# Kernel optimization log

Measured on AMD Instinct MI355X. Metric: run time of the kernel, lower is better.

Reference implementation:

```python
import jax, jax.numpy as jnp
import numpy as np

B, T, D, H = 2, 2048, 1024, 4
DK, DV = 1024, 2048          # key_dim = d_model*expand_k, value_dim = d_model*expand_v
HK, HV = DK // H, DV // H    # 256, 512 per-head dims
LR = 16                      # gate_low_rank_dim
EPS = 1e-5
GATE_NORM = 16.0             # gate_logit_normalizer


def _xavier(k, shape, gain):
    fan_in, fan_out = shape
    lim = gain * np.sqrt(6.0 / (fan_in + fan_out))
    return jax.random.uniform(k, shape, jnp.float32, -lim, lim)


def setup_inputs() -> dict:
    key = jax.random.key(0)
    ks = jax.random.split(key, 10)
    g_qkv = 2 ** (-2.5)
    return {
        "x": jax.random.normal(ks[0], (B, T, D), jnp.float32),
        "Wq": _xavier(ks[1], (D, DK), g_qkv),
        "Wk": _xavier(ks[2], (D, DK), g_qkv),
        "Wv": _xavier(ks[3], (D, DV), g_qkv),
        "Wg": _xavier(ks[4], (D, DV), g_qkv),
        "gk_w1": _xavier(ks[5], (D, LR), g_qkv),
        "gk_w2": _xavier(ks[6], (LR, DK), g_qkv),
        "gk_b": jnp.zeros((DK,), jnp.float32),
        "Wo": _xavier(ks[7], (DV, D), 2 ** (-1)),
        "rms_w": jnp.ones((HV,), jnp.float32),
    }


def _gla_scan(q, k, v, g):
    # q,k,g: [T, hk]; v: [T, hv]. Recurrence S_t = diag(exp(g_t)) S_{t-1} + k_t v_t^T; o_t = q_t @ S_t
    S0 = jnp.zeros((q.shape[-1], v.shape[-1]), q.dtype)

    def step(S, inp):
        qt, kt, vt, gt = inp
        S = jnp.exp(gt)[:, None] * S + kt[:, None] * vt[None, :]
        return S, qt @ S

    return jax.lax.scan(step, S0, (q, k, v, g))[1]  # [T, hv]


def _forward(x, Wq, Wk, Wv, Wg, gk_w1, gk_w2, gk_b, Wo, rms_w):
    b, t = x.shape[0], x.shape[1]
    scale = HK ** -0.5
    # projections -> [b, h, t, d_head]
    q = (x @ Wq).reshape(b, t, H, HK).transpose(0, 2, 1, 3) * scale
    k = (x @ Wk).reshape(b, t, H, HK).transpose(0, 2, 1, 3)
    v = (x @ Wv).reshape(b, t, H, HV).transpose(0, 2, 1, 3)
    # low-rank forget gate, log-space, fp32
    gl = (x @ gk_w1) @ gk_w2 + gk_b
    g = (jax.nn.log_sigmoid(gl.astype(jnp.float32)) / GATE_NORM)
    g = g.reshape(b, t, H, HK).transpose(0, 2, 1, 3)
    # per-(batch, head) linear-attention recurrence
    o = jax.vmap(jax.vmap(_gla_scan))(q, k, v, g)  # [b, h, t, hv]
    # group RMSNorm over head_v_dim
    o = o.transpose(0, 2, 1, 3)  # [b, t, h, hv]
    o = o * jax.lax.rsqrt(jnp.mean(o * o, axis=-1, keepdims=True) + EPS) * rms_w
    # output gate (swish) + out projection
    o = o.reshape(b, t, DV) * jax.nn.silu(x @ Wg)
    return o @ Wo  # [b, t, d_model]


def reference(x, Wq, Wk, Wv, Wg, gk_w1, gk_w2, gk_b, Wo, rms_w):
    return _forward(x, Wq, Wk, Wv, Wg, gk_w1, gk_w2, gk_b, Wo, rms_w)
```

## Files before the change

kernel.cpp:

```cpp
#include <hip/hip_runtime.h>
#include <cstdint>
#include <cstddef>


typedef unsigned short u16;
typedef __attribute__((ext_vector_type(8))) short s8v;
typedef __attribute__((ext_vector_type(4))) float f4v;

__device__ __forceinline__ u16 f2b(float f) {
  unsigned u = __builtin_bit_cast(unsigned, f);
  unsigned r = u + 0x7FFFu + ((u >> 16) & 1u);
  return (u16)(r >> 16);
}
__device__ __forceinline__ float b2f(u16 h) {
  unsigned u = ((unsigned)h) << 16;
  return __builtin_bit_cast(float, u);
}

__device__ __forceinline__ void cp16(const void* g, void* l) {
  __builtin_amdgcn_global_load_lds(
      (const __attribute__((address_space(1))) unsigned int*)g,
      (__attribute__((address_space(3))) unsigned int*)l, 16, 0, 0);
}

__device__ __forceinline__ void stage_tile(const u16* g, int ld, u16* lds,
                                           int wv, int ln) {
#pragma unroll
  for (int i = 0; i < 2; ++i) {
    const int c = wv * 2 + i;
    const u16* src = g + (size_t)(c * 16 + (ln >> 2)) * ld + (ln & 3) * 8;
    cp16(src, lds + c * 512);
  }
}

__device__ __forceinline__ void gemm_core(
    const u16* __restrict__ A, int lda, const u16* __restrict__ BT, int ldb,
    int K, u16* As, u16* Bs, f4v acc[4][4])
{
  const int tid = threadIdx.x;
  const int ln = tid & 63, wv = tid >> 6;
  const int arow = (wv >> 1) * 64 + (ln & 15);
  const int brow = (wv & 1) * 64 + (ln & 15);
  const int kq = (ln >> 4) * 8;
  const int nt = K >> 5;
  stage_tile(A, lda, As, wv, ln);
  stage_tile(BT, ldb, Bs, wv, ln);
  stage_tile(A + 32, lda, As + 4096, wv, ln);
  stage_tile(BT + 32, ldb, Bs + 4096, wv, ln);
  stage_tile(A + 64, lda, As + 8192, wv, ln);
  stage_tile(BT + 64, ldb, Bs + 8192, wv, ln);
  int slot = 0;
  for (int t = 0; t < nt; ++t) {
    const int rem = nt - 1 - t;
    if (rem >= 2)      asm volatile("s_waitcnt vmcnt(8)" ::: "memory");
    else if (rem == 1) asm volatile("s_waitcnt vmcnt(4)" ::: "memory");
    else               asm volatile("s_waitcnt vmcnt(0)" ::: "memory");
    __builtin_amdgcn_s_barrier();
    __builtin_amdgcn_sched_barrier(0);
    const u16* Ab = As + slot * 4096;
    const u16* Bb = Bs + slot * 4096;
    s8v af[4], bf[4];
#pragma unroll
    for (int f = 0; f < 4; ++f)
      af[f] = *(const s8v*)(Ab + (arow + f * 16) * 32 + kq);
#pragma unroll
    for (int f = 0; f < 4; ++f)
      bf[f] = *(const s8v*)(Bb + (brow + f * 16) * 32 + kq);
#pragma unroll
    for (int mf = 0; mf < 4; ++mf)
#pragma unroll
      for (int nf = 0; nf < 4; ++nf)
        acc[mf][nf] = __builtin_amdgcn_mfma_f32_16x16x32_bf16(
            af[mf], bf[nf], acc[mf][nf], 0, 0, 0);
    __builtin_amdgcn_sched_barrier(0);
    __builtin_amdgcn_s_barrier();
    if (t + 3 < nt) {
      stage_tile(A + (t + 3) * 32, lda, As + slot * 4096, wv, ln);
      stage_tile(BT + (t + 3) * 32, ldb, Bs + slot * 4096, wv, ln);
    }
    slot = (slot == 2) ? 0 : slot + 1;
  }
}

#define EPI_SETUP                                            \
  const int tid = threadIdx.x;                               \
  const int ln = tid & 63, wv = tid >> 6;                    \
  const int wr = wv >> 1, wc = wv & 1;

#define ZERO_ACC(acc)                                        \
  _Pragma("unroll")                                          \
  for (int zi = 0; zi < 4; ++zi)                             \
    _Pragma("unroll")                                        \
    for (int zj = 0; zj < 4; ++zj)                           \
      acc[zi][zj] = (f4v){0.f, 0.f, 0.f, 0.f};

__global__ __launch_bounds__(256) void cast_b(const float* __restrict__ in,
                                              u16* __restrict__ out) {
  const int i = blockIdx.x * 256 + threadIdx.x;
  const float4 v = ((const float4*)in)[i];
  u16* p = out + i * 4;
  p[0] = f2b(v.x); p[1] = f2b(v.y); p[2] = f2b(v.z); p[3] = f2b(v.w);
}

__global__ __launch_bounds__(256) void wtrans(const float* __restrict__ in,
                                              u16* __restrict__ out, int R, int C) {
  __shared__ float t[32][33];
  const int c0 = blockIdx.x * 32, r0 = blockIdx.y * 32;
  const int lx = threadIdx.x & 31, ly = threadIdx.x >> 5;
#pragma unroll
  for (int i = 0; i < 32; i += 8)
    t[ly + i][lx] = in[(size_t)(r0 + ly + i) * C + c0 + lx];
  __syncthreads();
#pragma unroll
  for (int i = 0; i < 32; i += 8)
    out[(size_t)(c0 + ly + i) * R + r0 + lx] = f2b(t[lx][ly + i]);
}

__global__ __launch_bounds__(256) void trans_b16(const u16* __restrict__ in,
                                                 u16* __restrict__ out, int R, int C) {
  __shared__ u16 t[32][33];
  const size_t boff = (size_t)blockIdx.z * R * C;
  const int c0 = blockIdx.x * 32, r0 = blockIdx.y * 32;
  const int lx = threadIdx.x & 31, ly = threadIdx.x >> 5;
#pragma unroll
  for (int i = 0; i < 32; i += 8)
    t[ly + i][lx] = in[boff + (size_t)(r0 + ly + i) * C + c0 + lx];
  __syncthreads();
#pragma unroll
  for (int i = 0; i < 32; i += 8)
    out[boff + (size_t)(c0 + ly + i) * R + r0 + lx] = t[lx][ly + i];
}

__global__ __launch_bounds__(256) void lowrank1(
    const float* __restrict__ x, const float* __restrict__ w1,
    float* __restrict__ tmp)
{
  const int idx = blockIdx.x * 256 + threadIdx.x;
  const int m = idx >> 4, i = idx & 15;
  const float* xr = x + (size_t)m * 1024;
  float acc = 0.f;
#pragma unroll 4
  for (int kk = 0; kk < 1024; kk += 4) {
    const float4 xv = *(const float4*)(xr + kk);
    acc = fmaf(xv.x, w1[(kk + 0) * 16 + i], acc);
    acc = fmaf(xv.y, w1[(kk + 1) * 16 + i], acc);
    acc = fmaf(xv.z, w1[(kk + 2) * 16 + i], acc);
    acc = fmaf(xv.w, w1[(kk + 3) * 16 + i], acc);
  }
  tmp[idx] = acc;
}

__global__ __launch_bounds__(256) void gate_cum(
    const float* __restrict__ tmp, const float* __restrict__ w2,
    const float* __restrict__ bias, u16* __restrict__ dq, u16* __restrict__ dk,
    float* __restrict__ Dc)
{
  __shared__ float ls_t[2048];
  const int b = blockIdx.y >> 4, c = blockIdx.y & 15;
  const int h = blockIdx.x;
  const int i = threadIdx.x;
  const int n = h * 256 + i;
  const int bh = b * 4 + h;
  const float* tp = tmp + ((size_t)(b * 2048 + c * 128)) * 16;
#pragma unroll
  for (int r = 0; r < 8; ++r) ls_t[r * 256 + threadIdx.x] = tp[r * 256 + threadIdx.x];
  __syncthreads();
  float w2c[16];
#pragma unroll
  for (int r = 0; r < 16; ++r) w2c[r] = w2[r * 1024 + n];
  const float bn = bias[n];
  const size_t base = ((size_t)bh * 2048 + c * 128) * 256 + i;
  float B = 0.f;
  for (int t = 0; t < 128; ++t) {
    float gl = bn;
    const float* tr = ls_t + t * 16;
#pragma unroll
    for (int r = 0; r < 16; ++r) gl = fmaf(tr[r], w2c[r], gl);
    const float ls = fminf(gl, 0.f) - log1pf(expf(-fabsf(gl)));
    B += ls * 0.0625f;
    const float eB = expf(B);
    dq[base + (size_t)t * 256] = f2b(eB);
    dk[base + (size_t)t * 256] = f2b(1.f / eB);
  }
  Dc[(bh * 16 + c) * 256 + i] = expf(B);
}

__global__ __launch_bounds__(256) void proj_all(
    const u16* __restrict__ xb, const u16* __restrict__ WT,
    const u16* __restrict__ dq, const u16* __restrict__ dk,
    u16* __restrict__ qt, u16* __restrict__ kt,
    u16* __restrict__ vr, u16* __restrict__ gpre)
{
  __shared__ __align__(16) u16 As[12288], Bs[12288];
  const int id = blockIdx.x;
  const int xcd = id & 7, j = id >> 3;
  const int m0 = (j / 6) * 128;
  const int n0 = (xcd * 6 + (j % 6)) * 128;
  f4v acc[4][4];
  ZERO_ACC(acc)
  gemm_core(xb + (size_t)m0 * 1024, 1024, WT + (size_t)n0 * 1024, 1024, 1024,
            As, Bs, acc);
  EPI_SETUP
#pragma unroll
  for (int mf = 0; mf < 4; ++mf)
#pragma unroll
    for (int nf = 0; nf < 4; ++nf)
#pragma unroll
      for (int r = 0; r < 4; ++r) {
        const int m = m0 + wr * 64 + mf * 16 + ((ln >> 4) << 2) + r;
        const int n = n0 + wc * 64 + nf * 16 + (ln & 15);
        const float val = acc[mf][nf][r];
        const int b = m >> 11, t = m & 2047;
        if (n0 < 1024) {
          const int bh = b * 4 + (n >> 8), i = n & 255;
          const size_t off = ((size_t)bh * 2048 + t) * 256 + i;
          qt[off] = f2b(val * 0.0625f * b2f(dq[off]));
        } else if (n0 < 2048) {
          const int nn = n - 1024;
          const int bh = b * 4 + (nn >> 8), i = nn & 255;
          const size_t off = ((size_t)bh * 2048 + t) * 256 + i;
          kt[off] = f2b(val * b2f(dk[off]));
        } else if (n0 < 4096) {
          const int nn = n - 2048;
          const int bh = b * 4 + (nn >> 9), jj = nn & 511;
          vr[((size_t)bh * 2048 + t) * 512 + jj] = f2b(val);
        } else {
          gpre[(size_t)m * 2048 + (n - 4096)] = f2b(val);
        }
      }
}

__global__ __launch_bounds__(256) void scan_gemms(
    const u16* __restrict__ vT, const u16* __restrict__ ktT,
    const u16* __restrict__ qt, const u16* __restrict__ kt,
    u16* __restrict__ UT, u16* __restrict__ Aw)
{
  __shared__ __align__(16) u16 As[12288], Bs[12288];
  const int bhc = blockIdx.y, bh = bhc >> 4, c = bhc & 15;
  f4v acc[4][4];
  ZERO_ACC(acc)
  if (blockIdx.x < 8) {
    const int mt = blockIdx.x >> 1, nt = blockIdx.x & 1;
    gemm_core(vT + ((size_t)bh * 512 + mt * 128) * 2048 + c * 128, 2048,
              ktT + ((size_t)bh * 256 + nt * 128) * 2048 + c * 128, 2048, 128,
              As, Bs, acc);
    EPI_SETUP
#pragma unroll
    for (int mf = 0; mf < 4; ++mf)
#pragma unroll
      for (int nf = 0; nf < 4; ++nf)
#pragma unroll
        for (int r = 0; r < 4; ++r) {
          const int j = mt * 128 + wr * 64 + mf * 16 + ((ln >> 4) << 2) + r;
          const int i = nt * 128 + wc * 64 + nf * 16 + (ln & 15);
          UT[(((size_t)(bh * 512 + j)) * 16 + c) * 256 + i] = f2b(acc[mf][nf][r]);
        }
  } else {
    const size_t base = ((size_t)bh * 2048 + c * 128) * 256;
    gemm_core(qt + base, 256, kt + base, 256, 256, As, Bs, acc);
    EPI_SETUP
    u16* Ap = Aw + (size_t)bhc * 16384;
#pragma unroll
    for (int mf = 0; mf < 4; ++mf)
#pragma unroll
      for (int nf = 0; nf < 4; ++nf)
#pragma unroll
        for (int r = 0; r < 4; ++r) {
          const int t = wr * 64 + mf * 16 + ((ln >> 4) << 2) + r;
          const int s = wc * 64 + nf * 16 + (ln & 15);
          Ap[t * 128 + s] = (s <= t) ? f2b(acc[mf][nf][r]) : (u16)0;
        }
  }
}

__global__ __launch_bounds__(256) void state_scan(
    u16* __restrict__ UT, const float* __restrict__ Dc)
{
  const int blk = blockIdx.x;
  const int bh = blk >> 9, j = blk & 511;
  const int i = threadIdx.x;
  u16* Up = UT + ((size_t)(bh * 512 + j)) * 16 * 256 + i;
  const float* Dp = Dc + bh * 16 * 256 + i;
  float S = 0.f;
  for (int c = 0; c < 16; ++c) {
    const float u = b2f(Up[c * 256]);
    Up[c * 256] = f2b(S);
    S = Dp[c * 256] * (S + u);
  }
}

__global__ __launch_bounds__(256) void intra_k(
    const u16* __restrict__ Aw, const u16* __restrict__ qt,
    const u16* __restrict__ vT, const u16* __restrict__ UT, u16* __restrict__ ob)
{
  __shared__ __align__(16) u16 As[12288], Bs[12288];
  const int jt = blockIdx.x;
  const int bhc = blockIdx.y, bh = bhc >> 4, c = bhc & 15;
  f4v acc[4][4];
  ZERO_ACC(acc)
  gemm_core(Aw + (size_t)bhc * 16384, 128,
            vT + ((size_t)bh * 512 + jt * 128) * 2048 + c * 128, 2048, 128,
            As, Bs, acc);
  gemm_core(qt + ((size_t)bh * 2048 + c * 128) * 256, 256,
            UT + ((size_t)(bh * 512 + jt * 128)) * 4096 + (size_t)c * 256, 4096, 256,
            As, Bs, acc);
  EPI_SETUP
  const int b = bh >> 2, h = bh & 3;
#pragma unroll
  for (int mf = 0; mf < 4; ++mf)
#pragma unroll
    for (int nf = 0; nf < 4; ++nf)
#pragma unroll
      for (int r = 0; r < 4; ++r) {
        const int t = c * 128 + wr * 64 + mf * 16 + ((ln >> 4) << 2) + r;
        const int j = jt * 128 + wc * 64 + nf * 16 + (ln & 15);
        ob[((size_t)(b * 2048 + t)) * 2048 + h * 512 + j] = f2b(acc[mf][nf][r]);
      }
}

__global__ __launch_bounds__(256) void rms_silu(
    u16* __restrict__ o, const u16* __restrict__ gpre, const float* __restrict__ w)
{
  const int grp = blockIdx.x * 4 + (threadIdx.x >> 6);
  const int lane = threadIdx.x & 63;
  const size_t base = (size_t)(grp >> 2) * 2048 + (grp & 3) * 512;
  float xv[8];
  float ss = 0.f;
#pragma unroll
  for (int i = 0; i < 8; ++i) {
    xv[i] = b2f(o[base + i * 64 + lane]);
    ss = fmaf(xv[i], xv[i], ss);
  }
#pragma unroll
  for (int off = 1; off < 64; off <<= 1) ss += __shfl_xor(ss, off, 64);
  const float r = rsqrtf(ss * (1.f / 512.f) + 1e-5f);
#pragma unroll
  for (int i = 0; i < 8; ++i) {
    const int cidx = i * 64 + lane;
    const float gp = b2f(gpre[base + cidx]);
    const float sig = 1.f / (1.f + expf(-gp));
    o[base + cidx] = f2b(xv[i] * r * w[cidx] * gp * sig);
  }
}

__global__ __launch_bounds__(256) void gemm_out(
    const u16* __restrict__ ob, const u16* __restrict__ WoT,
    float* __restrict__ pout)
{
  __shared__ __align__(16) u16 As[12288], Bs[12288];
  const int id = blockIdx.x;
  const int wg = (id & 7) * 64 + (id >> 3);
  const int ks = wg >> 8;
  const int tt = wg & 255;
  const int m0 = (tt & 31) * 128, n0 = (tt >> 5) * 128;
  f4v acc[4][4];
  ZERO_ACC(acc)
  gemm_core(ob + (size_t)m0 * 2048 + ks * 1024, 2048,
            WoT + (size_t)n0 * 2048 + ks * 1024, 2048, 1024, As, Bs, acc);
  EPI_SETUP
  float* po = pout + (size_t)ks * 4194304;
#pragma unroll
  for (int mf = 0; mf < 4; ++mf)
#pragma unroll
    for (int nf = 0; nf < 4; ++nf)
#pragma unroll
      for (int r = 0; r < 4; ++r) {
        const int m = m0 + wr * 64 + mf * 16 + ((ln >> 4) << 2) + r;
        const int n = n0 + wc * 64 + nf * 16 + (ln & 15);
        po[(size_t)m * 1024 + n] = acc[mf][nf][r];
      }
}

__global__ __launch_bounds__(256) void reduce_out(
    const float* __restrict__ p, float* __restrict__ out)
{
  const int i = blockIdx.x * 256 + threadIdx.x;
  const float4 a = ((const float4*)p)[i];
  const float4 b = ((const float4*)(p + 4194304))[i];
  ((float4*)out)[i] = make_float4(a.x + b.x, a.y + b.y, a.z + b.z, a.w + b.w);
}

extern "C" void kernel_launch(void* const* d_in, const int* in_sizes, int n_in,
                              void* d_out, int out_size, void* d_ws, size_t ws_size,
                              hipStream_t stream) {
  const float* x    = (const float*)d_in[0];
  const float* Wq   = (const float*)d_in[1];
  const float* Wk   = (const float*)d_in[2];
  const float* Wv   = (const float*)d_in[3];
  const float* Wg   = (const float*)d_in[4];
  const float* w1   = (const float*)d_in[5];
  const float* w2   = (const float*)d_in[6];
  const float* gb   = (const float*)d_in[7];
  const float* Wo   = (const float*)d_in[8];
  const float* rmsw = (const float*)d_in[9];
  float* out = (float*)d_out;

  char* W = (char*)d_ws;
  u16*   xb   = (u16*)W;   W += (size_t)8  << 20;
  u16*   WTa  = (u16*)W;   W += (size_t)12 << 20;
  u16*   WoT  = (u16*)W;   W += (size_t)4  << 20;
  u16*   qt   = (u16*)W;   W += (size_t)8  << 20;
  u16*   kt   = (u16*)W;   W += (size_t)8  << 20;
  u16*   vr   = (u16*)W;   W += (size_t)16 << 20;
  u16*   vT   = (u16*)W;   W += (size_t)16 << 20;
  u16*   ktT  = (u16*)W;   W += (size_t)8  << 20;
  u16*   gpre = (u16*)W;   W += (size_t)16 << 20;
  float* tmp  = (float*)W; W += (size_t)256 << 10;
  float* Dc   = (float*)W; W += (size_t)128 << 10;
  u16*   dq   = (u16*)W;   W += (size_t)8  << 20;
  u16*   dk   = (u16*)W;   W += (size_t)8  << 20;
  u16*   UT   = (u16*)W;   W += (size_t)32 << 20;
  u16*   Aw   = (u16*)W;   W += (size_t)4  << 20;
  u16*   ob   = (u16*)W;   W += (size_t)16 << 20;
  float* pout = (float*)W; W += (size_t)32 << 20;

  hipLaunchKernelGGL(lowrank1, dim3(256), dim3(256), 0, stream, x, w1, tmp);
  hipLaunchKernelGGL(gate_cum, dim3(4, 32), dim3(256), 0, stream,
                     tmp, w2, gb, dq, dk, Dc);

  hipLaunchKernelGGL(cast_b, dim3(4096), dim3(256), 0, stream, x, xb);
  hipLaunchKernelGGL(wtrans, dim3(32, 32), dim3(256), 0, stream, Wq, WTa, 1024, 1024);
  hipLaunchKernelGGL(wtrans, dim3(32, 32), dim3(256), 0, stream, Wk, WTa + 1048576, 1024, 1024);
  hipLaunchKernelGGL(wtrans, dim3(64, 32), dim3(256), 0, stream, Wv, WTa + 2097152, 1024, 2048);
  hipLaunchKernelGGL(wtrans, dim3(64, 32), dim3(256), 0, stream, Wg, WTa + 4194304, 1024, 2048);
  hipLaunchKernelGGL(wtrans, dim3(32, 64), dim3(256), 0, stream, Wo, WoT, 2048, 1024);

  hipLaunchKernelGGL(proj_all, dim3(1536), dim3(256), 0, stream,
                     xb, WTa, dq, dk, qt, kt, vr, gpre);

  hipLaunchKernelGGL(trans_b16, dim3(8, 64, 8), dim3(256), 0, stream,
                     kt, ktT, 2048, 256);
  hipLaunchKernelGGL(trans_b16, dim3(16, 64, 8), dim3(256), 0, stream,
                     vr, vT, 2048, 512);

  hipLaunchKernelGGL(scan_gemms, dim3(9, 128), dim3(256), 0, stream,
                     vT, ktT, qt, kt, UT, Aw);
  hipLaunchKernelGGL(state_scan, dim3(4096), dim3(256), 0, stream, UT, Dc);
  hipLaunchKernelGGL(intra_k, dim3(4, 128), dim3(256), 0, stream, Aw, qt, vT, UT, ob);

  hipLaunchKernelGGL(rms_silu, dim3(4096), dim3(256), 0, stream, ob, gpre, rmsw);
  hipLaunchKernelGGL(gemm_out, dim3(512), dim3(256), 0, stream, ob, WoT, pout);
  hipLaunchKernelGGL(reduce_out, dim3(4096), dim3(256), 0, stream, pout, out);
}
```

Baseline: 317.6 us.

## Swizzle GEMM LDS tiles and merge transpose launches into single kernels

The GEMM staging now permutes 16-byte chunks within each 32-element LDS row with an XOR swizzle, and the fragment reads use the matching swizzled offset. This is meant to cut LDS bank conflicts on the MFMA operand loads. Separately, the five weight-transpose launches and the two bf16 transpose launches are each folded into one kernel that dispatches on block index, which removes per-launch overhead. The swizzle has to agree exactly between the global-to-LDS copy and the reads, or the results will be wrong.

```diff
diff --git a/kernel.cpp b/kernel.cpp
--- a/kernel.cpp
+++ b/kernel.cpp
@@ -25,10 +25,11 @@
 
 __device__ __forceinline__ void stage_tile(const u16* g, int ld, u16* lds,
                                            int wv, int ln) {
+  const int q = (ln & 3) ^ ((ln >> 3) & 3);
 #pragma unroll
   for (int i = 0; i < 2; ++i) {
     const int c = wv * 2 + i;
-    const u16* src = g + (size_t)(c * 16 + (ln >> 2)) * ld + (ln & 3) * 8;
+    const u16* src = g + (size_t)(c * 16 + (ln >> 2)) * ld + q * 8;
     cp16(src, lds + c * 512);
   }
 }
@@ -41,7 +42,7 @@
   const int ln = tid & 63, wv = tid >> 6;
   const int arow = (wv >> 1) * 64 + (ln & 15);
   const int brow = (wv & 1) * 64 + (ln & 15);
-  const int kq = (ln >> 4) * 8;
+  const int koff = (((ln >> 4) ^ ((ln >> 1) & 3)) * 8);
   const int nt = K >> 5;
   stage_tile(A, lda, As, wv, ln);
   stage_tile(BT, ldb, Bs, wv, ln);
@@ -62,10 +63,10 @@
     s8v af[4], bf[4];
 #pragma unroll
     for (int f = 0; f < 4; ++f)
-      af[f] = *(const s8v*)(Ab + (arow + f * 16) * 32 + kq);
+      af[f] = *(const s8v*)(Ab + (arow + f * 16) * 32 + koff);
 #pragma unroll
     for (int f = 0; f < 4; ++f)
-      bf[f] = *(const s8v*)(Bb + (brow + f * 16) * 32 + kq);
+      bf[f] = *(const s8v*)(Bb + (brow + f * 16) * 32 + koff);
 #pragma unroll
     for (int mf = 0; mf < 4; ++mf)
 #pragma unroll
@@ -102,25 +103,43 @@
   p[0] = f2b(v.x); p[1] = f2b(v.y); p[2] = f2b(v.z); p[3] = f2b(v.w);
 }
 
-__global__ __launch_bounds__(256) void wtrans(const float* __restrict__ in,
-                                              u16* __restrict__ out, int R, int C) {
+__global__ __launch_bounds__(256) void wtrans_all(
+    const float* __restrict__ Wq, const float* __restrict__ Wk,
+    const float* __restrict__ Wv, const float* __restrict__ Wg,
+    const float* __restrict__ Wo, u16* __restrict__ WTa, u16* __restrict__ WoT)
+{
   __shared__ float t[32][33];
-  const int c0 = blockIdx.x * 32, r0 = blockIdx.y * 32;
+  const int id = blockIdx.x;
+  const float* src; u16* dst; int R, C, local;
+  if (id < 1024)      { src = Wq; dst = WTa;           R = 1024; C = 1024; local = id; }
+  else if (id < 2048) { src = Wk; dst = WTa + 1048576; R = 1024; C = 1024; local = id - 1024; }
+  else if (id < 4096) { src = Wv; dst = WTa + 2097152; R = 1024; C = 2048; local = id - 2048; }
+  else if (id < 6144) { src = Wg; dst = WTa + 4194304; R = 1024; C = 2048; local = id - 4096; }
+  else                { src = Wo; dst = WoT;           R = 2048; C = 1024; local = id - 6144; }
+  const int nx = C >> 5;
+  const int c0 = (local % nx) * 32, r0 = (local / nx) * 32;
   const int lx = threadIdx.x & 31, ly = threadIdx.x >> 5;
 #pragma unroll
   for (int i = 0; i < 32; i += 8)
-    t[ly + i][lx] = in[(size_t)(r0 + ly + i) * C + c0 + lx];
+    t[ly + i][lx] = src[(size_t)(r0 + ly + i) * C + c0 + lx];
   __syncthreads();
 #pragma unroll
   for (int i = 0; i < 32; i += 8)
-    out[(size_t)(c0 + ly + i) * R + r0 + lx] = f2b(t[lx][ly + i]);
-}
-
-__global__ __launch_bounds__(256) void trans_b16(const u16* __restrict__ in,
-                                                 u16* __restrict__ out, int R, int C) {
+    dst[(size_t)(c0 + ly + i) * R + r0 + lx] = f2b(t[lx][ly + i]);
+}
+
+__global__ __launch_bounds__(256) void trans_all(
+    const u16* __restrict__ kt, u16* __restrict__ ktT,
+    const u16* __restrict__ vr, u16* __restrict__ vT)
+{
   __shared__ u16 t[32][33];
-  const size_t boff = (size_t)blockIdx.z * R * C;
-  const int c0 = blockIdx.x * 32, r0 = blockIdx.y * 32;
+  const int id = blockIdx.x;
+  const u16* in; u16* out; int R = 2048, C, z, local;
+  if (id < 4096) { in = kt; out = ktT; C = 256;  z = id >> 9;  local = id & 511; }
+  else { const int i2 = id - 4096; in = vr; out = vT; C = 512; z = i2 >> 10; local = i2 & 1023; }
+  const int nx = C >> 5;
+  const int c0 = (local % nx) * 32, r0 = (local / nx) * 32;
+  const size_t boff = (size_t)z * R * C;
   const int lx = threadIdx.x & 31, ly = threadIdx.x >> 5;
 #pragma unroll
   for (int i = 0; i < 32; i += 8)
@@ -419,19 +438,14 @@
                      tmp, w2, gb, dq, dk, Dc);
 
   hipLaunchKernelGGL(cast_b, dim3(4096), dim3(256), 0, stream, x, xb);
-  hipLaunchKernelGGL(wtrans, dim3(32, 32), dim3(256), 0, stream, Wq, WTa, 1024, 1024);
-  hipLaunchKernelGGL(wtrans, dim3(32, 32), dim3(256), 0, stream, Wk, WTa + 1048576, 1024, 1024);
-  hipLaunchKernelGGL(wtrans, dim3(64, 32), dim3(256), 0, stream, Wv, WTa + 2097152, 1024, 2048);
-  hipLaunchKernelGGL(wtrans, dim3(64, 32), dim3(256), 0, stream, Wg, WTa + 4194304, 1024, 2048);
-  hipLaunchKernelGGL(wtrans, dim3(32, 64), dim3(256), 0, stream, Wo, WoT, 2048, 1024);
+  hipLaunchKernelGGL(wtrans_all, dim3(8192), dim3(256), 0, stream,
+                     Wq, Wk, Wv, Wg, Wo, WTa, WoT);
 
   hipLaunchKernelGGL(proj_all, dim3(1536), dim3(256), 0, stream,
                      xb, WTa, dq, dk, qt, kt, vr, gpre);
 
-  hipLaunchKernelGGL(trans_b16, dim3(8, 64, 8), dim3(256), 0, stream,
-                     kt, ktT, 2048, 256);
-  hipLaunchKernelGGL(trans_b16, dim3(16, 64, 8), dim3(256), 0, stream,
-                     vr, vT, 2048, 512);
+  hipLaunchKernelGGL(trans_all, dim3(12288), dim3(256), 0, stream,
+                     kt, ktT, vr, vT);
 
   hipLaunchKernelGGL(scan_gemms, dim3(9, 128), dim3(256), 0, stream,
                      vT, ktT, qt, kt, UT, Aw);
```

New measurement: 307.6 us. 3.1% less time.
